# Optimization experiments

Hardware: AMD Instinct MI355X
Metric: run time of the kernel (lower is better)

The kernel has to match this reference:

```python
import jax, jax.numpy as jnp
import numpy as np

B, T, H, LD = 32, 2048, 1024, 1024

def setup_inputs() -> dict:
    key = jax.random.key(0)
    k1, k2, k3, k4, k5 = jax.random.split(key, 5)
    scale = 1.0 / np.sqrt(H)
    return {
        "encoder_hidden": jax.random.normal(k1, (B, T, H), dtype=jnp.float32),
        "decoder_hidden": jax.random.normal(k2, (B, H), dtype=jnp.float32),
        "W1": jax.random.normal(k3, (H, LD), dtype=jnp.float32) * scale,
        "b1": jnp.zeros((LD,), dtype=jnp.float32),
        "W2": jax.random.normal(k4, (H, LD), dtype=jnp.float32) * scale,
        "b2": jnp.zeros((LD,), dtype=jnp.float32),
        "V": jax.random.normal(k5, (LD, 1), dtype=jnp.float32) * (1.0 / np.sqrt(LD)),
        "bV": jnp.zeros((1,), dtype=jnp.float32),
    }

def reference(encoder_hidden, decoder_hidden, W1, b1, W2, b2, V, bV):
    # dec proj: [B, 1, ld]
    dec_w = (decoder_hidden @ W1 + b1)[:, None, :]
    # enc proj: [B, T, ld]
    enc_w = jnp.einsum('bth,hl->btl', encoder_hidden, W2) + b2
    # multiplicative combine (as in source: decoder_Weight * encoder_weight)
    score = jnp.tanh(dec_w * enc_w) @ V + bV          # [B, T, 1]
    attn = jax.nn.softmax(score, axis=1)              # softmax over time
    context = jnp.sum(attn * encoder_hidden, axis=1)  # [B, H]
    return context, attn
```

## Files before the change

### kernel.cpp

```cpp
#include <hip/hip_runtime.h>
#include <hip/hip_bf16.h>
#include <math.h>

#define B_  32
#define T_  2048
#define H_  1024
#define LD_ 1024
#define M_  (B_*T_)

typedef __attribute__((ext_vector_type(8))) short bf16x8;
typedef __attribute__((ext_vector_type(4))) float f32x4;

__device__ __forceinline__ void async_copy16(void* lds, const void* g) {
  __builtin_amdgcn_global_load_lds(
      (const __attribute__((address_space(1))) void*)g,
      (__attribute__((address_space(3))) void*)lds, 16, 0, 0);
}

__global__ void convert_w2(const float* __restrict__ W2, __hip_bfloat16* __restrict__ w2p) {
  int idx = blockIdx.x * 256 + threadIdx.x;
  int kg = idx >> 10, n = idx & 1023;
  __align__(16) __hip_bfloat16 h[8];
#pragma unroll
  for (int j = 0; j < 8; ++j)
    h[j] = __float2bfloat16(W2[(size_t)(kg * 8 + j) * LD_ + n]);
  *reinterpret_cast<uint4*>(&w2p[(size_t)kg * (LD_ * 8) + n * 8]) =
      *reinterpret_cast<const uint4*>(h);
}

__global__ void dec_proj(const float* __restrict__ dec, const float* __restrict__ W1,
                         const float* __restrict__ b1, float* __restrict__ dec_w) {
  __shared__ float sdec[H_];
  int bb = blockIdx.x >> 2;
  int l = (blockIdx.x & 3) * 256 + threadIdx.x;
  for (int i = threadIdx.x; i < H_; i += 256) sdec[i] = dec[bb * H_ + i];
  __syncthreads();
  float a0 = 0.f, a1 = 0.f, a2 = 0.f, a3 = 0.f;
  for (int h = 0; h < H_; h += 4) {
    a0 += sdec[h + 0] * W1[(h + 0) * LD_ + l];
    a1 += sdec[h + 1] * W1[(h + 1) * LD_ + l];
    a2 += sdec[h + 2] * W1[(h + 2) * LD_ + l];
    a3 += sdec[h + 3] * W1[(h + 3) * LD_ + l];
  }
  dec_w[bb * LD_ + l] = (a0 + a1) + (a2 + a3) + b1[l];
}

__global__ __launch_bounds__(256, 2)
void score_gemm(const float* __restrict__ enc,
                const __hip_bfloat16* __restrict__ w2p,
                const float* __restrict__ dec_w,
                const float* __restrict__ b2,
                const float* __restrict__ V,
                float* __restrict__ score) {
  __shared__ __align__(16) __hip_bfloat16 Asm[4][128][8];
  __shared__ __align__(16) __hip_bfloat16 Bsm[4][256][8];

  const int tid  = threadIdx.x;
  const int lane = tid & 63;
  const int wave = tid >> 6;
  const int wm = wave >> 1, wn = wave & 1;
  const int nb = blockIdx.x, mb = blockIdx.y;
  const int row0 = mb * 128, col0 = nb * 256;
  const int q = lane >> 4, c15 = lane & 15;

  f32x4 acc[4][8] = {};

  const int sm  = tid >> 2;
  const int skg = tid & 3;

  for (int k0 = 0; k0 < H_; k0 += 32) {
#pragma unroll
    for (int pass = 0; pass < 2; ++pass) {
      int m = pass * 64 + sm;
      const float4* src = reinterpret_cast<const float4*>(
          enc + (size_t)(row0 + m) * H_ + k0 + skg * 8);
      float4 f0 = src[0], f1 = src[1];
      __align__(16) __hip_bfloat16 h[8];
      h[0] = __float2bfloat16(f0.x); h[1] = __float2bfloat16(f0.y);
      h[2] = __float2bfloat16(f0.z); h[3] = __float2bfloat16(f0.w);
      h[4] = __float2bfloat16(f1.x); h[5] = __float2bfloat16(f1.y);
      h[6] = __float2bfloat16(f1.z); h[7] = __float2bfloat16(f1.w);
      *reinterpret_cast<uint4*>(&Asm[skg][m][0]) = *reinterpret_cast<const uint4*>(h);
    }
    {
      char* bbase = (char*)&Bsm[0][0][0];
      const char* gbase = (const char*)w2p + ((size_t)(k0 >> 3)) * (LD_ * 8 * 2)
                          + (size_t)col0 * 16 + tid * 16;
#pragma unroll
      for (int p = 0; p < 4; ++p)
        async_copy16(bbase + p * 4096 + tid * 16, gbase + (size_t)p * (LD_ * 8 * 2));
    }
    __syncthreads();

    bf16x8 af[4], bfr[8];
#pragma unroll
    for (int i = 0; i < 4; ++i)
      af[i] = *reinterpret_cast<const bf16x8*>(&Asm[q][wm * 64 + i * 16 + c15][0]);
#pragma unroll
    for (int j = 0; j < 8; ++j)
      bfr[j] = *reinterpret_cast<const bf16x8*>(&Bsm[q][wn * 128 + j * 16 + c15][0]);
#pragma unroll
    for (int i = 0; i < 4; ++i)
#pragma unroll
      for (int j = 0; j < 8; ++j)
        acc[i][j] = __builtin_amdgcn_mfma_f32_16x16x32_bf16(af[i], bfr[j], acc[i][j], 0, 0, 0);
    __syncthreads();
  }

  const int bb = row0 >> 11;
  float b2v[8], dwv[8], Vv[8];
#pragma unroll
  for (int j = 0; j < 8; ++j) {
    int n = col0 + wn * 128 + j * 16 + c15;
    b2v[j] = b2[n];
    dwv[j] = dec_w[bb * LD_ + n];
    Vv[j]  = V[n];
  }
#pragma unroll
  for (int i = 0; i < 4; ++i) {
#pragma unroll
    for (int r = 0; r < 4; ++r) {
      float v = 0.f;
#pragma unroll
      for (int j = 0; j < 8; ++j) {
        float e = acc[i][j][r] + b2v[j];
        v += tanhf(dwv[j] * e) * Vv[j];
      }
      v += __shfl_xor(v, 1);
      v += __shfl_xor(v, 2);
      v += __shfl_xor(v, 4);
      v += __shfl_xor(v, 8);
      if (c15 == 0) {
        int row = row0 + wm * 64 + i * 16 + q * 4 + r;
        atomicAdd(&score[row], v);
      }
    }
  }
}

__global__ void softmax_k(const float* __restrict__ score, float* __restrict__ attn) {
  int bb = blockIdx.x;
  int tid = threadIdx.x;
  int lane = tid & 63, wave = tid >> 6;
  __shared__ float red[4];
  float v[8];
  float mx = -3.4e38f;
#pragma unroll
  for (int i = 0; i < 8; ++i) {
    v[i] = score[bb * T_ + i * 256 + tid];
    mx = fmaxf(mx, v[i]);
  }
#pragma unroll
  for (int m = 32; m >= 1; m >>= 1) mx = fmaxf(mx, __shfl_xor(mx, m));
  if (lane == 0) red[wave] = mx;
  __syncthreads();
  mx = fmaxf(fmaxf(red[0], red[1]), fmaxf(red[2], red[3]));
  __syncthreads();
  float s = 0.f;
#pragma unroll
  for (int i = 0; i < 8; ++i) { v[i] = __expf(v[i] - mx); s += v[i]; }
#pragma unroll
  for (int m = 32; m >= 1; m >>= 1) s += __shfl_xor(s, m);
  if (lane == 0) red[wave] = s;
  __syncthreads();
  s = red[0] + red[1] + red[2] + red[3];
  float inv = 1.f / s;
#pragma unroll
  for (int i = 0; i < 8; ++i) attn[bb * T_ + i * 256 + tid] = v[i] * inv;
}

__global__ void context_k(const float* __restrict__ enc, const float* __restrict__ attn,
                          float* __restrict__ ctx) {
  int bb = blockIdx.y;
  int hc = blockIdx.x & 3, tc = blockIdx.x >> 2;
  int h = hc * 256 + threadIdx.x;
  __shared__ float sat[512];
  int t0 = tc * 512;
  for (int i = threadIdx.x; i < 512; i += 256) sat[i] = attn[bb * T_ + t0 + i];
  __syncthreads();
  const float* base = enc + ((size_t)bb * T_ + t0) * H_ + h;
  float a0 = 0.f, a1 = 0.f, a2 = 0.f, a3 = 0.f;
  for (int t = 0; t < 512; t += 4) {
    a0 += sat[t + 0] * base[(size_t)(t + 0) * H_];
    a1 += sat[t + 1] * base[(size_t)(t + 1) * H_];
    a2 += sat[t + 2] * base[(size_t)(t + 2) * H_];
    a3 += sat[t + 3] * base[(size_t)(t + 3) * H_];
  }
  atomicAdd(&ctx[bb * H_ + h], (a0 + a1) + (a2 + a3));
}

extern "C" void kernel_launch(void* const* d_in, const int* in_sizes, int n_in,
                              void* d_out, int out_size, void* d_ws, size_t ws_size,
                              hipStream_t stream) {
  const float* enc = (const float*)d_in[0];
  const float* dec = (const float*)d_in[1];
  const float* W1  = (const float*)d_in[2];
  const float* b1  = (const float*)d_in[3];
  const float* W2  = (const float*)d_in[4];
  const float* b2  = (const float*)d_in[5];
  const float* V   = (const float*)d_in[6];

  char* ws = (char*)d_ws;
  __hip_bfloat16* w2p = (__hip_bfloat16*)ws;
  float* dec_w = (float*)(ws + (2u << 20));
  float* score = (float*)(ws + (2u << 20) + (128u << 10));

  float* out  = (float*)d_out;
  float* ctx  = out;
  float* attn = out + B_ * H_;

  hipMemsetAsync(score, 0, (size_t)M_ * sizeof(float), stream);
  hipMemsetAsync(ctx, 0, (size_t)B_ * H_ * sizeof(float), stream);

  convert_w2<<<(H_ * LD_ / 8) / 256, 256, 0, stream>>>(W2, w2p);
  dec_proj<<<B_ * 4, 256, 0, stream>>>(dec, W1, b1, dec_w);
  score_gemm<<<dim3(LD_ / 256, M_ / 128), 256, 0, stream>>>(enc, w2p, dec_w, b2, V, score);
  softmax_k<<<B_, 256, 0, stream>>>(score, attn);
  context_k<<<dim3(16, B_), 256, 0, stream>>>(enc, attn, ctx);
}
```

Before: 643.1 us.

## Load A fragments directly to registers and double-buffer B tiles in LDS

The score GEMM no longer stages the fp32 encoder tile through LDS. Each wave loads its own A fragment rows straight from global memory into registers and converts them to bf16 there. W2 tiles are double-buffered in LDS with asynchronous copies, and both A and B for the next k-step are prefetched while the current step's MFMAs run, leaving one barrier per iteration instead of two. The trade-offs are more registers for the prefetched A data, which can hurt the 2-blocks-per-CU occupancy. Because each wave now fetches its own A rows, the two waves that share a row range both read them from global memory, doubling A traffic.

New measurement: 723.3 us. 1.12x slower.

```diff
diff --git a/kernel.cpp b/kernel.cpp
--- a/kernel.cpp
+++ b/kernel.cpp
@@ -52,8 +52,7 @@
                 const float* __restrict__ b2,
                 const float* __restrict__ V,
                 float* __restrict__ score) {
-  __shared__ __align__(16) __hip_bfloat16 Asm[4][128][8];
-  __shared__ __align__(16) __hip_bfloat16 Bsm[4][256][8];
+  __shared__ __align__(16) __hip_bfloat16 Bsm[2][4][256][8];
 
   const int tid  = threadIdx.x;
   const int lane = tid & 63;
@@ -65,45 +64,65 @@
 
   f32x4 acc[4][8] = {};
 
-  const int sm  = tid >> 2;
-  const int skg = tid & 3;
-
+  const float* aptr[4];
+#pragma unroll
+  for (int i = 0; i < 4; ++i)
+    aptr[i] = enc + (size_t)(row0 + wm * 64 + i * 16 + c15) * H_ + q * 8;
+
+  char* bbase = (char*)&Bsm[0][0][0][0];
+  const char* gB = (const char*)w2p + (size_t)col0 * 16 + tid * 16;
+
+  float4 a0[4], a1[4];
+#pragma unroll
+  for (int i = 0; i < 4; ++i) {
+    const float4* p = reinterpret_cast<const float4*>(aptr[i]);
+    a0[i] = p[0]; a1[i] = p[1];
+  }
+#pragma unroll
+  for (int p4 = 0; p4 < 4; ++p4)
+    async_copy16(bbase + p4 * 4096 + tid * 16, gB + (size_t)p4 * 16384);
+  __syncthreads();
+
+#pragma unroll 2
   for (int k0 = 0; k0 < H_; k0 += 32) {
-#pragma unroll
-    for (int pass = 0; pass < 2; ++pass) {
-      int m = pass * 64 + sm;
-      const float4* src = reinterpret_cast<const float4*>(
-          enc + (size_t)(row0 + m) * H_ + k0 + skg * 8);
-      float4 f0 = src[0], f1 = src[1];
+    const int cur = (k0 >> 5) & 1, nxt = cur ^ 1;
+    const int kn = k0 + 32;
+    const int kp = (kn < H_) ? kn : 0;
+
+    float4 na0[4], na1[4];
+#pragma unroll
+    for (int i = 0; i < 4; ++i) {
+      const float4* p = reinterpret_cast<const float4*>(aptr[i] + kp);
+      na0[i] = p[0]; na1[i] = p[1];
+    }
+#pragma unroll
+    for (int p4 = 0; p4 < 4; ++p4)
+      async_copy16(bbase + nxt * 16384 + p4 * 4096 + tid * 16,
+                   gB + ((size_t)(kp >> 3) + p4) * 16384);
+
+    bf16x8 af[4];
+#pragma unroll
+    for (int i = 0; i < 4; ++i) {
       __align__(16) __hip_bfloat16 h[8];
-      h[0] = __float2bfloat16(f0.x); h[1] = __float2bfloat16(f0.y);
-      h[2] = __float2bfloat16(f0.z); h[3] = __float2bfloat16(f0.w);
-      h[4] = __float2bfloat16(f1.x); h[5] = __float2bfloat16(f1.y);
-      h[6] = __float2bfloat16(f1.z); h[7] = __float2bfloat16(f1.w);
-      *reinterpret_cast<uint4*>(&Asm[skg][m][0]) = *reinterpret_cast<const uint4*>(h);
-    }
-    {
-      char* bbase = (char*)&Bsm[0][0][0];
-      const char* gbase = (const char*)w2p + ((size_t)(k0 >> 3)) * (LD_ * 8 * 2)
-                          + (size_t)col0 * 16 + tid * 16;
-#pragma unroll
-      for (int p = 0; p < 4; ++p)
-        async_copy16(bbase + p * 4096 + tid * 16, gbase + (size_t)p * (LD_ * 8 * 2));
-    }
-    __syncthreads();
-
-    bf16x8 af[4], bfr[8];
-#pragma unroll
-    for (int i = 0; i < 4; ++i)
-      af[i] = *reinterpret_cast<const bf16x8*>(&Asm[q][wm * 64 + i * 16 + c15][0]);
-#pragma unroll
-    for (int j = 0; j < 8; ++j)
-      bfr[j] = *reinterpret_cast<const bf16x8*>(&Bsm[q][wn * 128 + j * 16 + c15][0]);
-#pragma unroll
-    for (int i = 0; i < 4; ++i)
-#pragma unroll
-      for (int j = 0; j < 8; ++j)
-        acc[i][j] = __builtin_amdgcn_mfma_f32_16x16x32_bf16(af[i], bfr[j], acc[i][j], 0, 0, 0);
+      h[0] = __float2bfloat16(a0[i].x); h[1] = __float2bfloat16(a0[i].y);
+      h[2] = __float2bfloat16(a0[i].z); h[3] = __float2bfloat16(a0[i].w);
+      h[4] = __float2bfloat16(a1[i].x); h[5] = __float2bfloat16(a1[i].y);
+      h[6] = __float2bfloat16(a1[i].z); h[7] = __float2bfloat16(a1[i].w);
+      af[i] = *reinterpret_cast<const bf16x8*>(h);
+    }
+
+#pragma unroll
+    for (int j = 0; j < 8; ++j) {
+      bf16x8 bfr = *reinterpret_cast<const bf16x8*>(
+          &Bsm[cur][q][wn * 128 + j * 16 + c15][0]);
+#pragma unroll
+      for (int i = 0; i < 4; ++i)
+        acc[i][j] = __builtin_amdgcn_mfma_f32_16x16x32_bf16(af[i], bfr, acc[i][j], 0, 0, 0);
+    }
+
+#pragma unroll
+    for (int i = 0; i < 4; ++i) { a0[i] = na0[i]; a1[i] = na1[i]; }
+
     __syncthreads();
   }
 
```

## Pre-convert encoder to tiled bf16 and async-load A tiles in score GEMM

Applied to the files above, without the earlier changes.

Adds a pre-pass that converts the fp32 encoder activations once into a tile-ordered bf16 buffer in workspace. The GEMM then loads both A and B tiles with async global-to-LDS copies. Previously each of the four column blocks re-read and re-converted the fp32 rows, so the GEMM fetched twice the bytes per tile and spent VALU time on conversion. The cost is an extra pass that reads 256MB and writes 128MB. The path only runs when the workspace is large enough, otherwise the old kernel is used.

Measured after the change: 672.3 us. 1.05x slower.

```diff
diff --git a/kernel.cpp b/kernel.cpp
--- a/kernel.cpp
+++ b/kernel.cpp
@@ -26,6 +26,32 @@
     h[j] = __float2bfloat16(W2[(size_t)(kg * 8 + j) * LD_ + n]);
   *reinterpret_cast<uint4*>(&w2p[(size_t)kg * (LD_ * 8) + n * 8]) =
       *reinterpret_cast<const uint4*>(h);
+}
+
+__global__ void convert_enc(const float* __restrict__ enc, __hip_bfloat16* __restrict__ encbf) {
+  __shared__ __align__(16) __hip_bfloat16 As[4][128][8];
+  const int ks = blockIdx.x, mb = blockIdx.y;
+  const int tid = threadIdx.x;
+  const int sm = tid >> 2, skg = tid & 3;
+  const int k0 = ks * 32;
+#pragma unroll
+  for (int pass = 0; pass < 2; ++pass) {
+    int m = pass * 64 + sm;
+    const float4* src = reinterpret_cast<const float4*>(
+        enc + (size_t)(mb * 128 + m) * H_ + k0 + skg * 8);
+    float4 f0 = src[0], f1 = src[1];
+    __align__(16) __hip_bfloat16 h[8];
+    h[0] = __float2bfloat16(f0.x); h[1] = __float2bfloat16(f0.y);
+    h[2] = __float2bfloat16(f0.z); h[3] = __float2bfloat16(f0.w);
+    h[4] = __float2bfloat16(f1.x); h[5] = __float2bfloat16(f1.y);
+    h[6] = __float2bfloat16(f1.z); h[7] = __float2bfloat16(f1.w);
+    *reinterpret_cast<uint4*>(&As[skg][m][0]) = *reinterpret_cast<const uint4*>(h);
+  }
+  __syncthreads();
+  const uint4* ls = reinterpret_cast<const uint4*>(&As[0][0][0]);
+  uint4* dst = reinterpret_cast<uint4*>(encbf) + (size_t)(mb * 32 + ks) * 512;
+  dst[tid]       = ls[tid];
+  dst[tid + 256] = ls[tid + 256];
 }
 
 __global__ void dec_proj(const float* __restrict__ dec, const float* __restrict__ W1,
@@ -46,12 +72,12 @@
 }
 
 __global__ __launch_bounds__(256, 2)
-void score_gemm(const float* __restrict__ enc,
-                const __hip_bfloat16* __restrict__ w2p,
-                const float* __restrict__ dec_w,
-                const float* __restrict__ b2,
-                const float* __restrict__ V,
-                float* __restrict__ score) {
+void score_gemm_t(const __hip_bfloat16* __restrict__ encbf,
+                  const __hip_bfloat16* __restrict__ w2p,
+                  const float* __restrict__ dec_w,
+                  const float* __restrict__ b2,
+                  const float* __restrict__ V,
+                  float* __restrict__ score) {
   __shared__ __align__(16) __hip_bfloat16 Asm[4][128][8];
   __shared__ __align__(16) __hip_bfloat16 Bsm[4][256][8];
 
@@ -65,9 +91,86 @@
 
   f32x4 acc[4][8] = {};
 
+  char* abase = (char*)&Asm[0][0][0];
+  char* bbase = (char*)&Bsm[0][0][0];
+  const char* gA = (const char*)encbf + (size_t)mb * (32 * 8192) + tid * 16;
+  const char* gB = (const char*)w2p + (size_t)col0 * 16 + tid * 16;
+
+  for (int k0 = 0; k0 < H_; k0 += 32) {
+    const int ks = k0 >> 5;
+    async_copy16(abase + tid * 16,        gA + (size_t)ks * 8192);
+    async_copy16(abase + tid * 16 + 4096, gA + (size_t)ks * 8192 + 4096);
+#pragma unroll
+    for (int p = 0; p < 4; ++p)
+      async_copy16(bbase + p * 4096 + tid * 16,
+                   gB + ((size_t)(k0 >> 3) + p) * 16384);
+    __syncthreads();
+
+    bf16x8 af[4], bfr[8];
+#pragma unroll
+    for (int i = 0; i < 4; ++i)
+      af[i] = *reinterpret_cast<const bf16x8*>(&Asm[q][wm * 64 + i * 16 + c15][0]);
+#pragma unroll
+    for (int j = 0; j < 8; ++j)
+      bfr[j] = *reinterpret_cast<const bf16x8*>(&Bsm[q][wn * 128 + j * 16 + c15][0]);
+#pragma unroll
+    for (int i = 0; i < 4; ++i)
+#pragma unroll
+      for (int j = 0; j < 8; ++j)
+        acc[i][j] = __builtin_amdgcn_mfma_f32_16x16x32_bf16(af[i], bfr[j], acc[i][j], 0, 0, 0);
+    __syncthreads();
+  }
+
+  const int bb = row0 >> 11;
+  float b2v[8], dwv[8], Vv[8];
+#pragma unroll
+  for (int j = 0; j < 8; ++j) {
+    int n = col0 + wn * 128 + j * 16 + c15;
+    b2v[j] = b2[n];
+    dwv[j] = dec_w[bb * LD_ + n];
+    Vv[j]  = V[n];
+  }
+#pragma unroll
+  for (int i = 0; i < 4; ++i) {
+#pragma unroll
+    for (int r = 0; r < 4; ++r) {
+      float v = 0.f;
+#pragma unroll
+      for (int j = 0; j < 8; ++j) {
+        float e = acc[i][j][r] + b2v[j];
+        v += tanhf(dwv[j] * e) * Vv[j];
+      }
+      v += __shfl_xor(v, 1);
+      v += __shfl_xor(v, 2);
+      v += __shfl_xor(v, 4);
+      v += __shfl_xor(v, 8);
+      if (c15 == 0) {
+        int row = row0 + wm * 64 + i * 16 + q * 4 + r;
+        atomicAdd(&score[row], v);
+      }
+    }
+  }
+}
+
+__global__ __launch_bounds__(256, 2)
+void score_gemm_f(const float* __restrict__ enc,
+                  const __hip_bfloat16* __restrict__ w2p,
+                  const float* __restrict__ dec_w,
+                  const float* __restrict__ b2,
+                  const float* __restrict__ V,
+                  float* __restrict__ score) {
+  __shared__ __align__(16) __hip_bfloat16 Asm[4][128][8];
+  __shared__ __align__(16) __hip_bfloat16 Bsm[4][256][8];
+  const int tid  = threadIdx.x;
+  const int lane = tid & 63;
+  const int wave = tid >> 6;
+  const int wm = wave >> 1, wn = wave & 1;
+  const int nb = blockIdx.x, mb = blockIdx.y;
+  const int row0 = mb * 128, col0 = nb * 256;
+  const int q = lane >> 4, c15 = lane & 15;
+  f32x4 acc[4][8] = {};
   const int sm  = tid >> 2;
   const int skg = tid & 3;
-
   for (int k0 = 0; k0 < H_; k0 += 32) {
 #pragma unroll
     for (int pass = 0; pass < 2; ++pass) {
@@ -91,7 +194,6 @@
         async_copy16(bbase + p * 4096 + tid * 16, gbase + (size_t)p * (LD_ * 8 * 2));
     }
     __syncthreads();
-
     bf16x8 af[4], bfr[8];
 #pragma unroll
     for (int i = 0; i < 4; ++i)
@@ -106,7 +208,6 @@
         acc[i][j] = __builtin_amdgcn_mfma_f32_16x16x32_bf16(af[i], bfr[j], acc[i][j], 0, 0, 0);
     __syncthreads();
   }
-
   const int bb = row0 >> 11;
   float b2v[8], dwv[8], Vv[8];
 #pragma unroll
@@ -204,6 +305,10 @@
   __hip_bfloat16* w2p = (__hip_bfloat16*)ws;
   float* dec_w = (float*)(ws + (2u << 20));
   float* score = (float*)(ws + (2u << 20) + (128u << 10));
+  __hip_bfloat16* encbf = (__hip_bfloat16*)(ws + (4ull << 20));
+
+  const size_t need = (4ull << 20) + (size_t)M_ * H_ * 2;
+  const bool tiled = ws_size >= need;
 
   float* out  = (float*)d_out;
   float* ctx  = out;
@@ -214,7 +319,12 @@
 
   convert_w2<<<(H_ * LD_ / 8) / 256, 256, 0, stream>>>(W2, w2p);
   dec_proj<<<B_ * 4, 256, 0, stream>>>(dec, W1, b1, dec_w);
-  score_gemm<<<dim3(LD_ / 256, M_ / 128), 256, 0, stream>>>(enc, w2p, dec_w, b2, V, score);
+  if (tiled) {
+    convert_enc<<<dim3(32, M_ / 128), 256, 0, stream>>>(enc, encbf);
+    score_gemm_t<<<dim3(LD_ / 256, M_ / 128), 256, 0, stream>>>(encbf, w2p, dec_w, b2, V, score);
+  } else {
+    score_gemm_f<<<dim3(LD_ / 256, M_ / 128), 256, 0, stream>>>(enc, w2p, dec_w, b2, V, score);
+  }
   softmax_k<<<B_, 256, 0, stream>>>(score, attn);
   context_k<<<dim3(16, B_), 256, 0, stream>>>(enc, attn, ctx);
 }
```
